# Performance work log

Measured on AMD Instinct MI355X. Metric: run time of the kernel, lower is better.

The kernel has to match this reference:

```python
import jax, jax.numpy as jnp
import numpy as np

B, T, C = 64, 256, 384
H, HD = 6, 64


def setup_inputs() -> dict:
    key = jax.random.key(0)
    ks = jax.random.split(key, 6)
    x = jax.random.normal(ks[0], (B, T, C), dtype=jnp.float32)
    s = 1.0 / np.sqrt(C)
    Wq = jax.random.normal(ks[1], (H, C, HD), dtype=jnp.float32) * s
    Wk = jax.random.normal(ks[2], (H, C, HD), dtype=jnp.float32) * s
    Wv = jax.random.normal(ks[3], (H, C, HD), dtype=jnp.float32) * s
    Wp = jax.random.normal(ks[4], (C, C), dtype=jnp.float32) * s
    bp = jnp.zeros((C,), dtype=jnp.float32)
    return {"x": x, "Wq": Wq, "Wk": Wk, "Wv": Wv, "Wp": Wp, "bp": bp}


def reference(x, Wq, Wk, Wv, Wp, bp):
    # per-head projections (no bias), vectorized over heads
    q = jnp.einsum('btc,hcd->bhtd', x, Wq)
    k = jnp.einsum('btc,hcd->bhtd', x, Wk)
    v = jnp.einsum('btc,hcd->bhtd', x, Wv)
    scale = HD ** (-0.5)
    scores = jnp.einsum('bhtd,bhsd->bhts', q, k) * scale  # [B,H,T,T]
    causal = jnp.tril(jnp.ones((T, T), dtype=bool))
    scores = jnp.where(causal, scores, -jnp.inf)
    wei = jax.nn.softmax(scores, axis=-1)  # dropout is identity in eval mode
    out = jnp.einsum('bhts,bhsd->bhtd', wei, v)
    out = out.transpose(0, 2, 1, 3).reshape(B, T, C)  # concat heads
    return out @ Wp.T + bp
```

## Files before the change

kernel.cpp:

```cpp
#include <hip/hip_runtime.h>
#include <hip/hip_bf16.h>
#include <cstdint>
#include <cstddef>

#define B_ 64
#define T_ 256
#define C_ 384
#define H_ 6
#define HD_ 64

using u16 = unsigned short;
typedef __attribute__((ext_vector_type(8))) short short8;
typedef __attribute__((ext_vector_type(4))) short short4_;
typedef __attribute__((ext_vector_type(4))) float f32x4;

__device__ __forceinline__ u16 f2bf(float f) {
    union { float f; uint32_t u; } x{f};
    uint32_t r = x.u + 0x7fffu + ((x.u >> 16) & 1u);
    return (u16)(r >> 16);
}

__global__ void k_prep(const float* __restrict__ x, const float* __restrict__ Wq,
                       const float* __restrict__ Wk, const float* __restrict__ Wv,
                       const float* __restrict__ Wp, u16* __restrict__ xb,
                       u16* __restrict__ wqkv, u16* __restrict__ wpb) {
    int bid = blockIdx.x;
    if (bid < 3072) {
        int i = (bid * 256 + threadIdx.x) * 8;
        const f32x4* p = (const f32x4*)(x + i);
        f32x4 a = p[0], b = p[1];
        short8 s;
        s[0] = (short)f2bf(a[0]); s[1] = (short)f2bf(a[1]);
        s[2] = (short)f2bf(a[2]); s[3] = (short)f2bf(a[3]);
        s[4] = (short)f2bf(b[0]); s[5] = (short)f2bf(b[1]);
        s[6] = (short)f2bf(b[2]); s[7] = (short)f2bf(b[3]);
        *(short8*)(xb + i) = s;
    } else if (bid < 3180) {
        __shared__ u16 Tt[64 * 65];
        int pb = bid - 3072;
        int which = pb / 36, rem = pb % 36;
        int h = rem / 6, cc0 = (rem % 6) * 64;
        const float* W = (which == 0) ? Wq : ((which == 1) ? Wk : Wv);
        int d = threadIdx.x & 63, cr0 = threadIdx.x >> 6;
#pragma unroll
        for (int p = 0; p < 16; ++p) {
            int cr = p * 4 + cr0;
            Tt[cr * 65 + d] = f2bf(W[(h * 384 + cc0 + cr) * 64 + d]);
        }
        __syncthreads();
        int ccl = threadIdx.x & 63, dl0 = threadIdx.x >> 6;
        int nbase = which * 384 + h * 64;
#pragma unroll
        for (int p = 0; p < 16; ++p) {
            int dl = p * 4 + dl0;
            wqkv[(size_t)(nbase + dl) * 384 + cc0 + ccl] = Tt[ccl * 65 + dl];
        }
    } else {
        int i = ((bid - 3180) * 256 + threadIdx.x) * 8;
        const f32x4* p = (const f32x4*)(Wp + i);
        f32x4 a = p[0], b = p[1];
        short8 s;
        s[0] = (short)f2bf(a[0]); s[1] = (short)f2bf(a[1]);
        s[2] = (short)f2bf(a[2]); s[3] = (short)f2bf(a[3]);
        s[4] = (short)f2bf(b[0]); s[5] = (short)f2bf(b[1]);
        s[6] = (short)f2bf(b[2]); s[7] = (short)f2bf(b[3]);
        *(short8*)(wpb + i) = s;
    }
}

template<int NROWS>
__device__ __forceinline__ void stage_rows(const u16* __restrict__ gbase, int ld,
                                           u16* lds_tile, int wid, int lane, int k0) {
#pragma unroll
    for (int i = 0; i < NROWS / 32; ++i) {
        int chunk = wid * (NROWS / 32) + i;
        int row = chunk * 8 + (lane >> 3);
        int pslot = lane & 7;
        const u16* gp = gbase + (size_t)row * ld + k0 + ((pslot ^ (row & 7)) << 3);
        u16* lp = lds_tile + chunk * 512;
        __builtin_amdgcn_global_load_lds((const __attribute__((address_space(1))) void*)gp,
                                         (__attribute__((address_space(3))) void*)lp, 16, 0, 0);
    }
}

__device__ __forceinline__ void stage_tile(const u16* __restrict__ gbase, int ld,
                                           u16* lds_tile, int wid, int lane, int k0) {
    stage_rows<128>(gbase, ld, lds_tile, wid, lane, k0);
}

__device__ __forceinline__ short8 read_frag(const u16* lds_tile, int row, int ks, int g) {
    int pslot = (ks * 4 + g) ^ (row & 7);
    return *(const short8*)&lds_tile[row * 64 + pslot * 8];
}

#define GEMM_PIPE_LOOP(NT)                                                        \
    int cur = 0;                                                                  \
    for (int t = 0; t < (NT); ++t) {                                              \
        if (t < (NT) - 1) {                                                       \
            stage_tile(Ag, 384, &lds[cur ^ 1][0], wid, lane, (t + 1) * 64);       \
            stage_tile(Bg, 384, &lds[cur ^ 1][8192], wid, lane, (t + 1) * 64);    \
            asm volatile("s_waitcnt vmcnt(8)" ::: "memory");                      \
        } else {                                                                  \
            asm volatile("s_waitcnt vmcnt(0)" ::: "memory");                      \
        }                                                                         \
        __builtin_amdgcn_s_barrier();                                             \
        __builtin_amdgcn_sched_barrier(0);                                        \
        const u16* A = &lds[cur][0];                                              \
        const u16* Bm = &lds[cur][8192];                                          \
        short8 af[2][4], bf[2][4];                                                \
        _Pragma("unroll")                                                         \
        for (int ks = 0; ks < 2; ++ks) {                                          \
            _Pragma("unroll")                                                     \
            for (int mf = 0; mf < 4; ++mf) af[ks][mf] = read_frag(A, wm * 64 + mf * 16 + c, ks, g); \
            _Pragma("unroll")                                                     \
            for (int nf = 0; nf < 4; ++nf) bf[ks][nf] = read_frag(Bm, wn * 64 + nf * 16 + c, ks, g); \
        }                                                                         \
        _Pragma("unroll")                                                         \
        for (int ks = 0; ks < 2; ++ks)                                            \
            _Pragma("unroll")                                                     \
            for (int mf = 0; mf < 4; ++mf)                                        \
                _Pragma("unroll")                                                 \
                for (int nf = 0; nf < 4; ++nf)                                    \
                    acc[mf][nf] = __builtin_amdgcn_mfma_f32_16x16x32_bf16(af[ks][mf], bf[ks][nf], acc[mf][nf], 0, 0, 0); \
        __builtin_amdgcn_sched_barrier(0);                                        \
        __builtin_amdgcn_s_barrier();                                             \
        cur ^= 1;                                                                 \
    }

__global__ __launch_bounds__(256, 2) void k_gemm_qkv(const u16* __restrict__ xb, const u16* __restrict__ wb,
                                                     u16* __restrict__ q, u16* __restrict__ k,
                                                     u16* __restrict__ v) {
    __shared__ alignas(16) u16 lds[2][16384];
    const int tid = threadIdx.x, lane = tid & 63, wid = tid >> 6;
    const int wm = wid >> 1, wn = wid & 1, g = lane >> 4, c = lane & 15;
    const int wg = blockIdx.x;
    const int xcd = wg & 7, q8 = wg >> 3;
    const int mj = (q8 / 9) * 8 + xcd;
    const int nk = q8 % 9;
    const int n0 = nk * 128, m0 = mj * 128;
    const u16* Ag = xb + (size_t)m0 * 384;
    const u16* Bg = wb + (size_t)n0 * 384;
    f32x4 acc[4][4] = {};
    stage_tile(Ag, 384, &lds[0][0], wid, lane, 0);
    stage_tile(Bg, 384, &lds[0][8192], wid, lane, 0);
    GEMM_PIPE_LOOP(6)
    const int which = n0 / 384;
    u16* dst = (which == 0) ? q : ((which == 1) ? k : v);
    const int h = ((n0 + wn * 64) % 384) / 64;
#pragma unroll
    for (int mf = 0; mf < 4; ++mf)
#pragma unroll
        for (int nf = 0; nf < 4; ++nf)
#pragma unroll
            for (int r = 0; r < 4; ++r) {
                int m = m0 + wm * 64 + mf * 16 + g * 4 + r;
                int d = nf * 16 + c;
                int b = m >> 8, t = m & 255;
                dst[((b * H_ + h) * T_ + t) * HD_ + d] = f2bf(acc[mf][nf][r]);
            }
}

__global__ __launch_bounds__(256, 2) void k_attn(const u16* __restrict__ q, const u16* __restrict__ k,
                                                 const u16* __restrict__ v, u16* __restrict__ ao) {
    __shared__ alignas(16) u16 Kl[2][64 * 64];
    __shared__ alignas(16) u16 Vt[2][64][72];
    const int tid = threadIdx.x, bh = blockIdx.x;
    const int lane = tid & 63, wid = tid >> 6;
    const int g = lane >> 4, c = lane & 15;
    const int bq = bh * 256;

    const int vd0 = (tid & 15) * 4;
    const int vs0 = (tid >> 4) * 4;
    const int kb0 = ((vs0 >> 5) << 5) | (((vs0 >> 2) & 3) << 3) | (((vs0 >> 4) & 1) << 2);

    short8 qB[4][2];
#pragma unroll
    for (int qf = 0; qf < 4; ++qf)
#pragma unroll
        for (int ks = 0; ks < 2; ++ks) {
            int t = wid * 64 + qf * 16 + c;
            qB[qf][ks] = *(const short8*)&q[(bq + t) * 64 + ks * 32 + g * 8];
        }
    float mrun[4], lrun[4];
#pragma unroll
    for (int i = 0; i < 4; ++i) { mrun[i] = -1e30f; lrun[i] = 0.f; }
    f32x4 o[4][4] = {};

    short4_ vv[4];
    stage_rows<64>(k + (size_t)(bq) * 64, 64, &Kl[0][0], wid, lane, 0);
#pragma unroll
    for (int i = 0; i < 4; ++i)
        vv[i] = *(const short4_*)&v[(size_t)(bq + vs0 + i) * 64 + vd0];
#pragma unroll
    for (int j = 0; j < 4; ++j) {
        short4_ w4;
#pragma unroll
        for (int i = 0; i < 4; ++i) w4[i] = vv[i][j];
        *(short4_*)&Vt[0][vd0 + j][kb0] = w4;
    }
    __syncthreads();

    int buf = 0;
    for (int kt = 0; kt < 4; ++kt) {
        if (kt < 3) {
            stage_rows<64>(k + (size_t)(bq + (kt + 1) * 64) * 64, 64, &Kl[buf ^ 1][0], wid, lane, 0);
#pragma unroll
            for (int i = 0; i < 4; ++i)
                vv[i] = *(const short4_*)&v[(size_t)(bq + (kt + 1) * 64 + vs0 + i) * 64 + vd0];
        }
        if (kt <= wid) {
            f32x4 st[4][4] = {};
            __builtin_amdgcn_s_setprio(1);
#pragma unroll
            for (int ks = 0; ks < 2; ++ks) {
                short8 kA[4];
#pragma unroll
                for (int sf = 0; sf < 4; ++sf)
                    kA[sf] = read_frag(&Kl[buf][0], sf * 16 + c, ks, g);
#pragma unroll
                for (int sf = 0; sf < 4; ++sf)
#pragma unroll
                    for (int qf = 0; qf < 4; ++qf)
                        st[sf][qf] = __builtin_amdgcn_mfma_f32_16x16x32_bf16(kA[sf], qB[qf][ks], st[sf][qf], 0, 0, 0);
            }
            __builtin_amdgcn_s_setprio(0);
            float pm[4] = {-1e30f, -1e30f, -1e30f, -1e30f};
#pragma unroll
            for (int sf = 0; sf < 4; ++sf)
#pragma unroll
                for (int qf = 0; qf < 4; ++qf)
#pragma unroll
                    for (int r = 0; r < 4; ++r) {
                        float val = st[sf][qf][r] * 0.125f;
                        if (kt == wid) {
                            int s_loc = sf * 16 + g * 4 + r, q_loc = qf * 16 + c;
                            if (s_loc > q_loc) val = -1e30f;
                        }
                        st[sf][qf][r] = val;
                        pm[qf] = fmaxf(pm[qf], val);
                    }
            float alpha[4];
#pragma unroll
            for (int qf = 0; qf < 4; ++qf) {
                pm[qf] = fmaxf(pm[qf], __shfl_xor(pm[qf], 16));
                pm[qf] = fmaxf(pm[qf], __shfl_xor(pm[qf], 32));
                float mnew = fmaxf(mrun[qf], pm[qf]);
                alpha[qf] = __expf(mrun[qf] - mnew);
                mrun[qf] = mnew;
            }
            short8 pA[4][2];
#pragma unroll
            for (int qf = 0; qf < 4; ++qf) {
                float ls = 0.f;
#pragma unroll
                for (int ks = 0; ks < 2; ++ks) {
                    short8 pa;
#pragma unroll
                    for (int half = 0; half < 2; ++half) {
                        f32x4 sv = st[2 * ks + half][qf];
#pragma unroll
                        for (int r = 0; r < 4; ++r) {
                            float p = __expf(sv[r] - mrun[qf]);
                            ls += p;
                            pa[half * 4 + r] = (short)f2bf(p);
                        }
                    }
                    pA[qf][ks] = pa;
                }
                ls += __shfl_xor(ls, 16);
                ls += __shfl_xor(ls, 32);
                lrun[qf] = lrun[qf] * alpha[qf] + ls;
            }
#pragma unroll
            for (int mf = 0; mf < 4; ++mf)
#pragma unroll
                for (int r = 0; r < 4; ++r) {
                    float aof = __shfl(alpha[mf], g * 4 + r);
#pragma unroll
                    for (int df = 0; df < 4; ++df)
                        o[mf][df][r] *= aof;
                }
            __builtin_amdgcn_s_setprio(1);
#pragma unroll
            for (int ks = 0; ks < 2; ++ks) {
                short8 vB[4];
#pragma unroll
                for (int df = 0; df < 4; ++df)
                    vB[df] = *(short8*)&Vt[buf][df * 16 + c][ks * 32 + g * 8];
#pragma unroll
                for (int mf = 0; mf < 4; ++mf)
#pragma unroll
                    for (int df = 0; df < 4; ++df)
                        o[mf][df] = __builtin_amdgcn_mfma_f32_16x16x32_bf16(pA[mf][ks], vB[df], o[mf][df], 0, 0, 0);
            }
            __builtin_amdgcn_s_setprio(0);
        }
        if (kt < 3) {
#pragma unroll
            for (int j = 0; j < 4; ++j) {
                short4_ w4;
#pragma unroll
                for (int i = 0; i < 4; ++i) w4[i] = vv[i][j];
                *(short4_*)&Vt[buf ^ 1][vd0 + j][kb0] = w4;
            }
        }
        __syncthreads();
        buf ^= 1;
    }
    const int bb = bh / H_, hh = bh % H_;
#pragma unroll
    for (int mf = 0; mf < 4; ++mf)
#pragma unroll
        for (int r = 0; r < 4; ++r) {
            float inv = 1.0f / __shfl(lrun[mf], g * 4 + r);
            int t = wid * 64 + mf * 16 + g * 4 + r;
#pragma unroll
            for (int df = 0; df < 4; ++df) {
                int d = df * 16 + c;
                ao[((size_t)(bb * T_ + t)) * C_ + hh * 64 + d] = f2bf(o[mf][df][r] * inv);
            }
        }
}

__global__ __launch_bounds__(256, 2) void k_gemm_proj(const u16* __restrict__ ab, const u16* __restrict__ wp,
                                                      const float* __restrict__ bp, float* __restrict__ out) {
    __shared__ alignas(16) u16 lds[2][16384];
    const int tid = threadIdx.x, lane = tid & 63, wid = tid >> 6;
    const int wm = wid >> 1, wn = wid & 1, g = lane >> 4, c = lane & 15;
    const int wg = blockIdx.x;
    const int xcd = wg & 7, q8 = wg >> 3;
    const int mj = (q8 / 3) * 8 + xcd;
    const int nk = q8 % 3;
    const int n0 = nk * 128, m0 = mj * 128;
    const u16* Ag = ab + (size_t)m0 * 384;
    const u16* Bg = wp + (size_t)n0 * 384;
    f32x4 acc[4][4] = {};
    stage_tile(Ag, 384, &lds[0][0], wid, lane, 0);
    stage_tile(Bg, 384, &lds[0][8192], wid, lane, 0);
    GEMM_PIPE_LOOP(6)
#pragma unroll
    for (int mf = 0; mf < 4; ++mf)
#pragma unroll
        for (int nf = 0; nf < 4; ++nf)
#pragma unroll
            for (int r = 0; r < 4; ++r) {
                int m = m0 + wm * 64 + mf * 16 + g * 4 + r;
                int n = n0 + wn * 64 + nf * 16 + c;
                out[(size_t)m * C_ + n] = acc[mf][nf][r] + bp[n];
            }
}


extern "C" void kernel_launch(void* const* d_in, const int* in_sizes, int n_in,
                              void* d_out, int out_size, void* d_ws, size_t ws_size,
                              hipStream_t stream) {
    const float* x  = (const float*)d_in[0];
    const float* Wq = (const float*)d_in[1];
    const float* Wk = (const float*)d_in[2];
    const float* Wv = (const float*)d_in[3];
    const float* Wp = (const float*)d_in[4];
    const float* bp = (const float*)d_in[5];
    float* out = (float*)d_out;

    char* ws = (char*)d_ws;
    u16* xb   = (u16*)(ws);
    u16* wqkv = (u16*)(ws + 12582912);
    u16* wpb  = (u16*)(ws + 13467648);
    u16* qb   = (u16*)(ws + 13762560);
    u16* kb   = (u16*)(ws + 26345472);
    u16* vb   = (u16*)(ws + 38928384);
    u16* ab   = (u16*)(ws + 51511296);

    k_prep<<<3252, 256, 0, stream>>>(x, Wq, Wk, Wv, Wp, xb, wqkv, wpb);
    k_gemm_qkv<<<1152, 256, 0, stream>>>(xb, wqkv, qb, kb, vb);
    k_attn<<<384, 256, 0, stream>>>(qb, kb, vb, ab);
    k_gemm_proj<<<384, 256, 0, stream>>>(ab, wpb, bp, out);
}
```

Measured before the change: 65.91 us.

## Interleave query row tiles across waves to balance causal attention work

Each wave now owns query fragments strided across the sequence (qf*4+wid) instead of a contiguous 64-row block, so every wave does a similar amount of work under the causal mask. Previously wave 3 did four key tiles while wave 0 did one, leaving waves idle at each barrier. The key-tile loop is fully unrolled so buffer indices and the skipped fragments become compile-time constants. This raises register pressure and code size.

```diff
diff --git a/kernel.cpp b/kernel.cpp
--- a/kernel.cpp
+++ b/kernel.cpp
@@ -178,7 +178,7 @@
     for (int qf = 0; qf < 4; ++qf)
 #pragma unroll
         for (int ks = 0; ks < 2; ++ks) {
-            int t = wid * 64 + qf * 16 + c;
+            int t = (qf * 4 + wid) * 16 + c;
             qB[qf][ks] = *(const short8*)&q[(bq + t) * 64 + ks * 32 + g * 8];
         }
     float mrun[4], lrun[4];
@@ -200,15 +200,16 @@
     }
     __syncthreads();
 
-    int buf = 0;
+#pragma unroll
     for (int kt = 0; kt < 4; ++kt) {
+        const int buf = kt & 1;
         if (kt < 3) {
             stage_rows<64>(k + (size_t)(bq + (kt + 1) * 64) * 64, 64, &Kl[buf ^ 1][0], wid, lane, 0);
 #pragma unroll
             for (int i = 0; i < 4; ++i)
                 vv[i] = *(const short4_*)&v[(size_t)(bq + (kt + 1) * 64 + vs0 + i) * 64 + vd0];
         }
-        if (kt <= wid) {
+        {
             f32x4 st[4][4] = {};
             __builtin_amdgcn_s_setprio(1);
 #pragma unroll
@@ -220,28 +221,29 @@
 #pragma unroll
                 for (int sf = 0; sf < 4; ++sf)
 #pragma unroll
-                    for (int qf = 0; qf < 4; ++qf)
+                    for (int qf = kt; qf < 4; ++qf)
                         st[sf][qf] = __builtin_amdgcn_mfma_f32_16x16x32_bf16(kA[sf], qB[qf][ks], st[sf][qf], 0, 0, 0);
             }
             __builtin_amdgcn_s_setprio(0);
-            float pm[4] = {-1e30f, -1e30f, -1e30f, -1e30f};
+            float pm[4];
+#pragma unroll
+            for (int qf = kt; qf < 4; ++qf) pm[qf] = -1e30f;
 #pragma unroll
             for (int sf = 0; sf < 4; ++sf)
 #pragma unroll
-                for (int qf = 0; qf < 4; ++qf)
+                for (int qf = kt; qf < 4; ++qf)
 #pragma unroll
                     for (int r = 0; r < 4; ++r) {
                         float val = st[sf][qf][r] * 0.125f;
-                        if (kt == wid) {
-                            int s_loc = sf * 16 + g * 4 + r, q_loc = qf * 16 + c;
-                            if (s_loc > q_loc) val = -1e30f;
+                        if (qf == kt) {
+                            if (sf * 16 + g * 4 + r > 16 * wid + c) val = -1e30f;
                         }
                         st[sf][qf][r] = val;
                         pm[qf] = fmaxf(pm[qf], val);
                     }
             float alpha[4];
 #pragma unroll
-            for (int qf = 0; qf < 4; ++qf) {
+            for (int qf = kt; qf < 4; ++qf) {
                 pm[qf] = fmaxf(pm[qf], __shfl_xor(pm[qf], 16));
                 pm[qf] = fmaxf(pm[qf], __shfl_xor(pm[qf], 32));
                 float mnew = fmaxf(mrun[qf], pm[qf]);
@@ -250,7 +252,7 @@
             }
             short8 pA[4][2];
 #pragma unroll
-            for (int qf = 0; qf < 4; ++qf) {
+            for (int qf = kt; qf < 4; ++qf) {
                 float ls = 0.f;
 #pragma unroll
                 for (int ks = 0; ks < 2; ++ks) {
@@ -272,13 +274,13 @@
                 lrun[qf] = lrun[qf] * alpha[qf] + ls;
             }
 #pragma unroll
-            for (int mf = 0; mf < 4; ++mf)
+            for (int qf = kt; qf < 4; ++qf)
 #pragma unroll
                 for (int r = 0; r < 4; ++r) {
-                    float aof = __shfl(alpha[mf], g * 4 + r);
+                    float aof = __shfl(alpha[qf], g * 4 + r);
 #pragma unroll
                     for (int df = 0; df < 4; ++df)
-                        o[mf][df][r] *= aof;
+                        o[qf][df][r] *= aof;
                 }
             __builtin_amdgcn_s_setprio(1);
 #pragma unroll
@@ -288,10 +290,10 @@
                 for (int df = 0; df < 4; ++df)
                     vB[df] = *(short8*)&Vt[buf][df * 16 + c][ks * 32 + g * 8];
 #pragma unroll
-                for (int mf = 0; mf < 4; ++mf)
+                for (int qf = kt; qf < 4; ++qf)
 #pragma unroll
                     for (int df = 0; df < 4; ++df)
-                        o[mf][df] = __builtin_amdgcn_mfma_f32_16x16x32_bf16(pA[mf][ks], vB[df], o[mf][df], 0, 0, 0);
+                        o[qf][df] = __builtin_amdgcn_mfma_f32_16x16x32_bf16(pA[qf][ks], vB[df], o[qf][df], 0, 0, 0);
             }
             __builtin_amdgcn_s_setprio(0);
         }
@@ -305,19 +307,18 @@
             }
         }
         __syncthreads();
-        buf ^= 1;
     }
     const int bb = bh / H_, hh = bh % H_;
 #pragma unroll
-    for (int mf = 0; mf < 4; ++mf)
+    for (int qf = 0; qf < 4; ++qf)
 #pragma unroll
         for (int r = 0; r < 4; ++r) {
-            float inv = 1.0f / __shfl(lrun[mf], g * 4 + r);
-            int t = wid * 64 + mf * 16 + g * 4 + r;
+            float inv = 1.0f / __shfl(lrun[qf], g * 4 + r);
+            int t = (qf * 4 + wid) * 16 + g * 4 + r;
 #pragma unroll
             for (int df = 0; df < 4; ++df) {
                 int d = df * 16 + c;
-                ao[((size_t)(bb * T_ + t)) * C_ + hh * 64 + d] = f2bf(o[mf][df][r] * inv);
+                ao[((size_t)(bb * T_ + t)) * C_ + hh * 64 + d] = f2bf(o[qf][df][r] * inv);
             }
         }
 }
```

After: 61.87 us, median of 4. 1.07x faster.
